# Kernel optimization log

Hardware: AMD Instinct MI355X
Metric: run time of the kernel (lower is better)

## Reference

```python
import jax, jax.numpy as jnp
import numpy as np

B, NIN, D = 2048, 64, 128
N_LCB, N_FMB, RANK = 32, 32, 24
DIM_HIDDEN = 1024
N_OUT = N_LCB + N_FMB  # == NIN -> identity residual
MAX_VAL = 1.0
EPS_LN_FMB_MIN, EPS_LN_FMB_MAX = 1e-11, 1e7
KERAS_LN_EPS = 1e-3


def setup_inputs() -> dict:
    key = jax.random.key(0)
    ks = jax.random.split(key, 9)
    def w(k, shape, fan):
        return (jax.random.normal(k, shape, jnp.float32) / np.sqrt(fan)).astype(jnp.float32)
    return {
        "x": jax.random.normal(ks[0], (B, NIN, D), jnp.float32),
        "noise": jax.random.uniform(ks[1], (B, N_OUT, D), jnp.float32),
        "w_lcb": w(ks[2], (NIN, N_LCB), NIN),
        "w_rank": w(ks[3], (NIN, RANK), NIN),
        "w1": w(ks[4], (NIN * RANK, DIM_HIDDEN), NIN * RANK),
        "w2": w(ks[5], (DIM_HIDDEN, DIM_HIDDEN), DIM_HIDDEN),
        "w3": w(ks[6], (DIM_HIDDEN, N_FMB * D), DIM_HIDDEN),
        "gamma": jnp.ones((D,), jnp.float32),
        "beta": jnp.zeros((D,), jnp.float32),
    }


def _forward(x, noise, w_lcb, w_rank, w1, w2, w3, gamma, beta):
    # ---- LinearCompressBlock: Dense over feature (emb-count) axis ----
    lcb = jnp.einsum("bnd,nm->bmd", x, w_lcb)  # (B, N_LCB, D)

    # ---- FactorizationMachineBlock ----
    # rank_layer on transposed input: (B, D, NIN) @ (NIN, RANK)
    r = jnp.einsum("bnd,nr->bdr", x, w_rank)          # (B, D, RANK)
    fm = jnp.einsum("bnd,bdr->bnr", x, r)             # (B, NIN, RANK)
    fm = fm.reshape(fm.shape[0], NIN * RANK)
    # custom LayerNorm (no affine, clipped std)
    mu = jnp.mean(fm, axis=-1, keepdims=True)
    cen = fm - mu
    std = jnp.sqrt(jnp.mean(cen * cen, axis=-1, keepdims=True))
    std = jnp.clip(std, EPS_LN_FMB_MIN, EPS_LN_FMB_MAX)
    fm = cen / std
    # MLP: 2 hidden relu layers + linear out, dropout=0 / inference
    h = jax.nn.relu(fm @ w1)
    h = jax.nn.relu(h @ w2)
    fmb = (h @ w3).reshape(-1, N_FMB, D)              # (B, N_FMB, D)

    out = jnp.concatenate((fmb, lcb), axis=1)          # (B, N_OUT, D)
    residual = x                                        # NIN == N_OUT -> identity

    safe = jnp.clip(out, -MAX_VAL, MAX_VAL)
    a = jnp.abs(safe)
    c = lambda t: jnp.clip(t, -MAX_VAL, MAX_VAL)

    # conv term: reshape to (B, N, D//8, 8), 1x1 conv with all-ones (8->8)
    # filter == group-sum broadcast back over the 8 lanes
    g = safe.reshape(safe.shape[0], N_OUT, D // 8, 8)
    conv = jnp.broadcast_to(g.sum(-1, keepdims=True), g.shape).reshape(safe.shape)

    extra = (
        c(jnp.log(a + 1.0))
        + c(jax.lax.rsqrt(a + 1.0))
        + c(jax.nn.softmax(safe, axis=-1))
        + c(jnp.tanh(safe))
        + c(jnp.where(safe >= 0, safe, 0.2 * safe))          # leaky_relu alpha=0.2
        + c(jnp.exp(safe))
        + c(jax.nn.softplus(safe))
        + c(jnp.log1p(a))
        + jnp.zeros_like(safe)                               # zeros_like term
        + c(jnp.round(safe))
        + jnp.ones_like(safe)                                # pow(a+eps, 0) == 1
        + c(jnp.sign(safe))
        + c(jnp.prod(safe, axis=-1, keepdims=True))
        + c(jnp.isnan(safe).astype(jnp.float32))
        + c((~(safe < 0)).astype(jnp.float32))
        + c((safe != 0).astype(jnp.float32))
        + c((safe >= 0).astype(jnp.float32))
        + c(safe.astype(jnp.int8).astype(jnp.float32))       # bitwise_and(x,x)==x after int8 cast
        + c(jnp.max(safe, axis=-1, keepdims=True))
        + c(safe + safe)                                     # add_n([safe, safe])
        + c(safe + safe)                                     # raw Add
        + 7.0 * safe                                         # slice/split-concat/merge/einsum/squeeze/pad/stack identities (|safe|<=1 so clip no-op)
        + c(jnp.where(safe > 0.5, -1.0, safe))               # tensor_scatter_nd_update
        + c(conv)
        + c(noise)                                           # tf.random.uniform (deterministic input)
        + c(jnp.arange(D, dtype=jnp.float32))                # broadcast over last axis
        + c(jnp.sum(safe[0] * safe[0], axis=-1))[None, :, None]  # DiagPart(matmul(safe[0], safe[0]^T))
    )

    pre = out + residual + 1e-10 * extra
    # keras LayerNormalization(axis=-1), default epsilon=1e-3
    m = jnp.mean(pre, axis=-1, keepdims=True)
    v = jnp.mean(jnp.square(pre - m), axis=-1, keepdims=True)
    return (pre - m) * jax.lax.rsqrt(v + KERAS_LN_EPS) * gamma + beta


def reference(x, noise, w_lcb, w_rank, w1, w2, w3, gamma, beta):
    return _forward(x, noise, w_lcb, w_rank, w1, w2, w3, gamma, beta)
```

## Files before the change

### kernel.cpp

```cpp
#include <hip/hip_runtime.h>


typedef _Float16 half8_t __attribute__((ext_vector_type(8)));
typedef _Float16 half4_t __attribute__((ext_vector_type(4)));
typedef float floatx4 __attribute__((ext_vector_type(4)));

#define B_SZ 2048
#define NIN 64
#define D_SZ 128
#define RANK 24
#define FMK (NIN * RANK)
#define HID 1024
#define NFMB_D (32 * 128)
#define ROW_F (NIN * D_SZ)

__global__ __launch_bounds__(256) void transpose_cast_all(
    const float* __restrict__ w1, const float* __restrict__ w2,
    const float* __restrict__ w3, const float* __restrict__ w_rank,
    const float* __restrict__ w_lcb, _Float16* __restrict__ w1t,
    _Float16* __restrict__ w2t, _Float16* __restrict__ w3t,
    _Float16* __restrict__ wr16, _Float16* __restrict__ wl16) {
  __shared__ float tile[32][33];
  int bid = blockIdx.x;
  if (bid == 48 * 32 + 32 * 32 + 32 * 128) {
    const int t = threadIdx.x;
#pragma unroll
    for (int k = 0; k < 8; k++) {
      int i = t + k * 256;
      int j = i >> 6, n = i & 63;
      wr16[i] = (_Float16)(j < RANK ? w_rank[n * RANK + j] : 0.f);
      wl16[i] = (_Float16)w_lcb[n * 32 + j];
    }
    return;
  }
  const float* w;
  _Float16* wt;
  int K, N, kt;
  if (bid < 48 * 32) {
    w = w1; wt = w1t; K = FMK; N = HID; kt = 48;
  } else if (bid < 48 * 32 + 32 * 32) {
    bid -= 48 * 32;
    w = w2; wt = w2t; K = HID; N = HID; kt = 32;
  } else {
    bid -= 48 * 32 + 32 * 32;
    w = w3; wt = w3t; K = HID; N = NFMB_D; kt = 32;
  }
  const int tk = (bid % kt) * 32;
  const int tn = (bid / kt) * 32;
  const int tx = threadIdx.x & 31;
  const int ty = threadIdx.x >> 5;
#pragma unroll
  for (int i = 0; i < 4; i++) {
    int k = ty + i * 8;
    tile[k][tx] = w[(size_t)(tk + k) * N + (tn + tx)];
  }
  __syncthreads();
#pragma unroll
  for (int i = 0; i < 4; i++) {
    int n = ty + i * 8;
    wt[(size_t)(tn + n) * K + (tk + tx)] = (_Float16)tile[tx][n];
  }
}

#define STX 72
#define STN 136
__global__ __launch_bounds__(256, 3) void front_kernel(
    const float* __restrict__ x, const _Float16* __restrict__ wr16,
    const _Float16* __restrict__ wl16, const float* __restrict__ gamma,
    const float* __restrict__ beta, _Float16* __restrict__ fmn,
    float* __restrict__ out) {
  constexpr int XT_OFF = 0;
  constexpr int X16_OFF = 18432;
  constexpr int RT_OFF = X16_OFF + 17408;
  constexpr int RED_OFF = RT_OFF + 8704;
  __shared__ __align__(16) char smem[RED_OFF + 32];
  __shared__ float2 lstat[32][4];
  _Float16* xT = (_Float16*)(smem + XT_OFF);
  _Float16* x16 = (_Float16*)(smem + X16_OFF);
  _Float16* rT = (_Float16*)(smem + RT_OFF);
  float* redbuf = (float*)(smem + RED_OFF);
  _Float16* fmn_s = (_Float16*)(smem + RT_OFF);

  const int b = blockIdx.x, t = threadIdx.x;
  const int lane = t & 63;
  const int w = __builtin_amdgcn_readfirstlane(t >> 6);
  const int q = lane >> 4, ln = lane & 15;

  half8_t ar[2][2], al[2][2];
#pragma unroll
  for (int k = 0; k < 2; k++)
#pragma unroll
    for (int mi = 0; mi < 2; mi++) {
      ar[k][mi] = *(const half8_t*)&wr16[(mi * 16 + ln) * 64 + k * 32 + q * 8];
      al[k][mi] = *(const half8_t*)&wl16[(mi * 16 + ln) * 64 + k * 32 + q * 8];
    }

  const float4* xg4 = (const float4*)(x + (size_t)b * ROW_F);
#pragma unroll
  for (int hh = 0; hh < 2; hh++) {
    int bb = t + hh * 256;
    int n0 = (bb >> 5) * 4;
    int bd = bb & 31;
    int d0 = bd * 4;
    float4 L0 = xg4[(n0 + 0) * 32 + bd];
    float4 L1 = xg4[(n0 + 1) * 32 + bd];
    float4 L2 = xg4[(n0 + 2) * 32 + bd];
    float4 L3 = xg4[(n0 + 3) * 32 + bd];
    *(half4_t*)&x16[(n0 + 0) * STN + d0] =
        half4_t{(_Float16)L0.x, (_Float16)L0.y, (_Float16)L0.z, (_Float16)L0.w};
    *(half4_t*)&x16[(n0 + 1) * STN + d0] =
        half4_t{(_Float16)L1.x, (_Float16)L1.y, (_Float16)L1.z, (_Float16)L1.w};
    *(half4_t*)&x16[(n0 + 2) * STN + d0] =
        half4_t{(_Float16)L2.x, (_Float16)L2.y, (_Float16)L2.z, (_Float16)L2.w};
    *(half4_t*)&x16[(n0 + 3) * STN + d0] =
        half4_t{(_Float16)L3.x, (_Float16)L3.y, (_Float16)L3.z, (_Float16)L3.w};
    *(half4_t*)&xT[(d0 + 0) * STX + n0] =
        half4_t{(_Float16)L0.x, (_Float16)L1.x, (_Float16)L2.x, (_Float16)L3.x};
    *(half4_t*)&xT[(d0 + 1) * STX + n0] =
        half4_t{(_Float16)L0.y, (_Float16)L1.y, (_Float16)L2.y, (_Float16)L3.y};
    *(half4_t*)&xT[(d0 + 2) * STX + n0] =
        half4_t{(_Float16)L0.z, (_Float16)L1.z, (_Float16)L2.z, (_Float16)L3.z};
    *(half4_t*)&xT[(d0 + 3) * STX + n0] =
        half4_t{(_Float16)L0.w, (_Float16)L1.w, (_Float16)L2.w, (_Float16)L3.w};
  }
  __syncthreads();

  floatx4 r_acc[2][2] = {};
  floatx4 l_acc[2][2] = {};
#pragma unroll
  for (int k = 0; k < 2; k++) {
    half8_t bfrag[2];
#pragma unroll
    for (int ni = 0; ni < 2; ni++)
      bfrag[ni] =
          *(const half8_t*)&xT[((2 * w + ni) * 16 + ln) * STX + k * 32 + q * 8];
#pragma unroll
    for (int mi = 0; mi < 2; mi++)
#pragma unroll
      for (int ni = 0; ni < 2; ni++) {
        r_acc[mi][ni] = __builtin_amdgcn_mfma_f32_16x16x32_f16(
            ar[k][mi], bfrag[ni], r_acc[mi][ni], 0, 0, 0);
        l_acc[mi][ni] = __builtin_amdgcn_mfma_f32_16x16x32_f16(
            al[k][mi], bfrag[ni], l_acc[mi][ni], 0, 0, 0);
      }
  }
#pragma unroll
  for (int mi = 0; mi < 2; mi++)
#pragma unroll
    for (int ni = 0; ni < 2; ni++)
#pragma unroll
      for (int rr = 0; rr < 4; rr++)
        rT[(mi * 16 + q * 4 + rr) * STN + (2 * w + ni) * 16 + ln] =
            (_Float16)r_acc[mi][ni][rr];
  __syncthreads();

  floatx4 f_acc[2] = {};
#pragma unroll
  for (int k = 0; k < 4; k++) {
    half8_t af = *(const half8_t*)&x16[(w * 16 + ln) * STN + k * 32 + q * 8];
#pragma unroll
    for (int nj = 0; nj < 2; nj++) {
      half8_t bf = *(const half8_t*)&rT[(nj * 16 + ln) * STN + k * 32 + q * 8];
      f_acc[nj] =
          __builtin_amdgcn_mfma_f32_16x16x32_f16(af, bf, f_acc[nj], 0, 0, 0);
    }
  }
  float s = 0.f, s2 = 0.f;
#pragma unroll
  for (int rr = 0; rr < 4; rr++) {
    float v = f_acc[0][rr];
    s += v;
    s2 += v * v;
    float v1 = (ln < 8) ? f_acc[1][rr] : 0.f;
    s += v1;
    s2 += v1 * v1;
  }
#pragma unroll
  for (int off = 1; off < 64; off <<= 1) {
    s += __shfl_xor(s, off);
    s2 += __shfl_xor(s2, off);
  }
  if (lane == 0) {
    redbuf[w * 2] = s;
    redbuf[w * 2 + 1] = s2;
  }
  __syncthreads();
  s = redbuf[0] + redbuf[2] + redbuf[4] + redbuf[6];
  s2 = redbuf[1] + redbuf[3] + redbuf[5] + redbuf[7];
  const float mu = s * (1.f / FMK);
  float var = s2 * (1.f / FMK) - mu * mu;
  var = var > 0.f ? var : 0.f;
  float sd = sqrtf(var);
  sd = sd < 1e-11f ? 1e-11f : (sd > 1e7f ? 1e7f : sd);
  const float inv = 1.f / sd;

#pragma unroll
  for (int nj = 0; nj < 2; nj++) {
    int j = nj * 16 + ln;
    if (j < RANK) {
#pragma unroll
      for (int rr = 0; rr < 4; rr++)
        fmn_s[(w * 16 + q * 4 + rr) * RANK + j] =
            (_Float16)((f_acc[nj][rr] - mu) * inv);
    }
  }

  const int d0 = (2 * w) * 16 + ln;
  const int d1 = d0 + 16;
  const float g0 = gamma[d0], g1 = gamma[d1];
  const float be0 = beta[d0], be1 = beta[d1];
  float lv0[2][4], lv1[2][4];
  float sw[2][4], s2w[2][4];
#pragma unroll
  for (int mi = 0; mi < 2; mi++)
#pragma unroll
    for (int rr = 0; rr < 4; rr++) {
      int m = mi * 16 + q * 4 + rr;
      float v0 = l_acc[mi][0][rr] + (float)x16[(32 + m) * STN + d0];
      float v1 = l_acc[mi][1][rr] + (float)x16[(32 + m) * STN + d1];
      lv0[mi][rr] = v0;
      lv1[mi][rr] = v1;
      sw[mi][rr] = v0 + v1;
      s2w[mi][rr] = v0 * v0 + v1 * v1;
    }
#pragma unroll
  for (int off = 1; off < 16; off <<= 1) {
#pragma unroll
    for (int mi = 0; mi < 2; mi++)
#pragma unroll
      for (int rr = 0; rr < 4; rr++) {
        sw[mi][rr] += __shfl_xor(sw[mi][rr], off);
        s2w[mi][rr] += __shfl_xor(s2w[mi][rr], off);
      }
  }
  if (ln == 0) {
#pragma unroll
    for (int mi = 0; mi < 2; mi++)
#pragma unroll
      for (int rr = 0; rr < 4; rr++)
        lstat[mi * 16 + q * 4 + rr][w] = float2{sw[mi][rr], s2w[mi][rr]};
  }
  __syncthreads();

  half8_t* fg = (half8_t*)(fmn + (size_t)b * FMK);
  if (t < FMK / 8) fg[t] = ((const half8_t*)fmn_s)[t];
  float* ob = out + (size_t)b * ROW_F;
#pragma unroll
  for (int mi = 0; mi < 2; mi++)
#pragma unroll
    for (int rr = 0; rr < 4; rr++) {
      int m = mi * 16 + q * 4 + rr;
      float2 p0 = lstat[m][0], p1 = lstat[m][1];
      float2 p2 = lstat[m][2], p3 = lstat[m][3];
      float S = p0.x + p1.x + p2.x + p3.x;
      float S2 = p0.y + p1.y + p2.y + p3.y;
      float mean = S * (1.f / 128.f);
      float varr = S2 * (1.f / 128.f) - mean * mean;
      float rstd = rsqrtf(varr + 1e-3f);
      ob[(32 + m) * 128 + d0] = (lv0[mi][rr] - mean) * rstd * g0 + be0;
      ob[(32 + m) * 128 + d1] = (lv1[mi][rr] - mean) * rstd * g1 + be1;
    }
}

template <int MT, bool RELU>
__global__ __launch_bounds__(256, 2) void gemm_bt(
    const _Float16* __restrict__ A, const _Float16* __restrict__ Bt,
    _Float16* __restrict__ C, int M, int N, int K) {
  constexpr int LDT = 40;
  constexpr int MI = MT / 32;
  __shared__ __align__(16) _Float16 As[MT * LDT];
  __shared__ __align__(16) _Float16 Bs[128 * LDT];
  const int m0 = blockIdx.x * MT;
  const int n0 = blockIdx.y * 128;
  const int t = threadIdx.x;
  const int wave = t >> 6, lane = t & 63;
  const int wr = wave >> 1, wc = wave & 1;
  const int q = lane >> 4, ln = lane & 15;
  const int srow = t >> 2;
  const int skc = t & 3;
  const _Float16* gA0 = A + (size_t)(m0 + srow) * K + skc * 8;
  const _Float16* gA1 = gA0 + (size_t)64 * K;
  const _Float16* gB0 = Bt + (size_t)(n0 + srow) * K + skc * 8;
  const _Float16* gB1 = gB0 + (size_t)64 * K;
  const int ldsw = srow * LDT + skc * 8;

  floatx4 acc[MI][4] = {};

  uint4 ra0 = *(const uint4*)(gA0);
  uint4 ra1;
  if constexpr (MT == 128) ra1 = *(const uint4*)(gA1);
  uint4 rb0 = *(const uint4*)(gB0);
  uint4 rb1 = *(const uint4*)(gB1);

  for (int k0 = 0;;) {
    __syncthreads();
    *(uint4*)&As[ldsw] = ra0;
    if constexpr (MT == 128) *(uint4*)&As[64 * LDT + ldsw] = ra1;
    *(uint4*)&Bs[ldsw] = rb0;
    *(uint4*)&Bs[64 * LDT + ldsw] = rb1;
    __syncthreads();
    k0 += 32;
    if (k0 < K) {
      ra0 = *(const uint4*)(gA0 + k0);
      if constexpr (MT == 128) ra1 = *(const uint4*)(gA1 + k0);
      rb0 = *(const uint4*)(gB0 + k0);
      rb1 = *(const uint4*)(gB1 + k0);
    }
    half8_t af[MI], bf[4];
#pragma unroll
    for (int i = 0; i < MI; i++)
      af[i] = *(const half8_t*)&As[(wr * (MT / 2) + i * 16 + ln) * LDT + q * 8];
#pragma unroll
    for (int j = 0; j < 4; j++)
      bf[j] = *(const half8_t*)&Bs[(wc * 64 + j * 16 + ln) * LDT + q * 8];
#pragma unroll
    for (int i = 0; i < MI; i++)
#pragma unroll
      for (int j = 0; j < 4; j++)
        acc[i][j] =
            __builtin_amdgcn_mfma_f32_16x16x32_f16(af[i], bf[j], acc[i][j], 0, 0, 0);
    if (k0 >= K) break;
  }

#pragma unroll
  for (int i = 0; i < MI; i++) {
#pragma unroll
    for (int r = 0; r < 4; r++) {
      size_t row = (size_t)(m0 + wr * (MT / 2) + i * 16 + q * 4 + r);
      _Float16* crow = C + row * N + n0 + wc * 64 + ln;
#pragma unroll
      for (int j = 0; j < 4; j++) {
        float v = acc[i][j][r];
        if (RELU) v = v > 0.f ? v : 0.f;
        crow[j * 16] = (_Float16)v;
      }
    }
  }
}

__global__ __launch_bounds__(256, 2) void gemm_ln(
    const _Float16* __restrict__ A, const _Float16* __restrict__ Bt,
    const float* __restrict__ x, const float* __restrict__ gamma,
    const float* __restrict__ beta, float* __restrict__ out) {
  constexpr int LDT = 40;
  constexpr int LDXS = 132;
  constexpr int K = HID;
  __shared__ __align__(16) _Float16 As[128 * LDT];
  __shared__ __align__(16) _Float16 Bs[128 * LDT];
  __shared__ __align__(16) _Float16 xs[128 * LDXS];
  __shared__ float2 rowst[128][2];
  const int m0 = blockIdx.x * 128;
  const int c = blockIdx.y;
  const int n0 = c * 128;
  const int t = threadIdx.x;
  const int wave = t >> 6, lane = t & 63;
  const int wr = wave >> 1, wc = wave & 1;
  const int q = lane >> 4, ln = lane & 15;
  const int srow = t >> 2;
  const int skc = t & 3;
  const _Float16* gA0 = A + (size_t)(m0 + srow) * K + skc * 8;
  const _Float16* gA1 = gA0 + (size_t)64 * K;
  const _Float16* gB0 = Bt + (size_t)(n0 + srow) * K + skc * 8;
  const _Float16* gB1 = gB0 + (size_t)64 * K;
  const int ldsw = srow * LDT + skc * 8;

  floatx4 acc[4][4] = {};
  uint4 ra0 = *(const uint4*)(gA0);
  uint4 ra1 = *(const uint4*)(gA1);
  uint4 rb0 = *(const uint4*)(gB0);
  uint4 rb1 = *(const uint4*)(gB1);

  for (int k0 = 0;;) {
    __syncthreads();
    *(uint4*)&As[ldsw] = ra0;
    *(uint4*)&As[64 * LDT + ldsw] = ra1;
    *(uint4*)&Bs[ldsw] = rb0;
    *(uint4*)&Bs[64 * LDT + ldsw] = rb1;
    __syncthreads();
    k0 += 32;
    if (k0 < K) {
      ra0 = *(const uint4*)(gA0 + k0);
      ra1 = *(const uint4*)(gA1 + k0);
      rb0 = *(const uint4*)(gB0 + k0);
      rb1 = *(const uint4*)(gB1 + k0);
    }
    half8_t af[4], bf[4];
#pragma unroll
    for (int i = 0; i < 4; i++)
      af[i] = *(const half8_t*)&As[(wr * 64 + i * 16 + ln) * LDT + q * 8];
#pragma unroll
    for (int j = 0; j < 4; j++)
      bf[j] = *(const half8_t*)&Bs[(wc * 64 + j * 16 + ln) * LDT + q * 8];
#pragma unroll
    for (int i = 0; i < 4; i++)
#pragma unroll
      for (int j = 0; j < 4; j++)
        acc[i][j] =
            __builtin_amdgcn_mfma_f32_16x16x32_f16(af[i], bf[j], acc[i][j], 0, 0, 0);
    if (k0 >= K) break;
  }

#pragma unroll
  for (int ii = 0; ii < 16; ii++) {
    int idx = t + ii * 256;
    int row = idx >> 5, f4 = idx & 31;
    float4 v = *(const float4*)(x + (size_t)(m0 + row) * ROW_F + n0 + f4 * 4);
    *(half4_t*)&xs[row * LDXS + f4 * 4] =
        half4_t{(_Float16)v.x, (_Float16)v.y, (_Float16)v.z, (_Float16)v.w};
  }
  __syncthreads();

  float s[4][4], s2[4][4];
#pragma unroll
  for (int i = 0; i < 4; i++)
#pragma unroll
    for (int r = 0; r < 4; r++) {
      int row = wr * 64 + i * 16 + q * 4 + r;
      float ss = 0.f, qq = 0.f;
#pragma unroll
      for (int j = 0; j < 4; j++) {
        float v = acc[i][j][r] + (float)xs[row * LDXS + wc * 64 + j * 16 + ln];
        acc[i][j][r] = v;
        ss += v;
        qq += v * v;
      }
      s[i][r] = ss;
      s2[i][r] = qq;
    }
#pragma unroll
  for (int off = 1; off < 16; off <<= 1) {
#pragma unroll
    for (int i = 0; i < 4; i++)
#pragma unroll
      for (int r = 0; r < 4; r++) {
        s[i][r] += __shfl_xor(s[i][r], off);
        s2[i][r] += __shfl_xor(s2[i][r], off);
      }
  }
  if (ln == 0) {
#pragma unroll
    for (int i = 0; i < 4; i++)
#pragma unroll
      for (int r = 0; r < 4; r++)
        rowst[wr * 64 + i * 16 + q * 4 + r][wc] = float2{s[i][r], s2[i][r]};
  }
  __syncthreads();
  float g[4], bb[4];
#pragma unroll
  for (int j = 0; j < 4; j++) {
    g[j] = gamma[wc * 64 + j * 16 + ln];
    bb[j] = beta[wc * 64 + j * 16 + ln];
  }
#pragma unroll
  for (int i = 0; i < 4; i++)
#pragma unroll
    for (int r = 0; r < 4; r++) {
      int row = wr * 64 + i * 16 + q * 4 + r;
      float2 p0 = rowst[row][0], p1 = rowst[row][1];
      float mean = (p0.x + p1.x) * (1.f / 128.f);
      float varr = (p0.y + p1.y) * (1.f / 128.f) - mean * mean;
      float rstd = rsqrtf(varr + 1e-3f);
      float* orow = out + (size_t)(m0 + row) * ROW_F + n0 + wc * 64 + ln;
#pragma unroll
      for (int j = 0; j < 4; j++)
        orow[j * 16] = (acc[i][j][r] - mean) * rstd * g[j] + bb[j];
    }
}

extern "C" void kernel_launch(void* const* d_in, const int* in_sizes, int n_in,
                              void* d_out, int out_size, void* d_ws,
                              size_t ws_size, hipStream_t stream) {
  const float* x = (const float*)d_in[0];
  const float* w_lcb = (const float*)d_in[2];
  const float* w_rank = (const float*)d_in[3];
  const float* w1 = (const float*)d_in[4];
  const float* w2 = (const float*)d_in[5];
  const float* w3 = (const float*)d_in[6];
  const float* gamma = (const float*)d_in[7];
  const float* beta = (const float*)d_in[8];
  float* out = (float*)d_out;

  char* ws = (char*)d_ws;
  _Float16* w1t = (_Float16*)ws; ws += (size_t)HID * FMK * 2;
  _Float16* w2t = (_Float16*)ws; ws += (size_t)HID * HID * 2;
  _Float16* w3t = (_Float16*)ws; ws += (size_t)NFMB_D * HID * 2;
  _Float16* fmn = (_Float16*)ws; ws += (size_t)B_SZ * FMK * 2;
  _Float16* h1  = (_Float16*)ws; ws += (size_t)B_SZ * HID * 2;
  _Float16* wr16 = (_Float16*)ws; ws += 32 * 64 * 2;
  _Float16* wl16 = (_Float16*)ws; ws += 32 * 64 * 2;
  _Float16* h2 = fmn;

  transpose_cast_all<<<48 * 32 + 32 * 32 + 32 * 128 + 1, 256, 0, stream>>>(
      w1, w2, w3, w_rank, w_lcb, w1t, w2t, w3t, wr16, wl16);
  front_kernel<<<B_SZ, 256, 0, stream>>>(x, wr16, wl16, gamma, beta, fmn, out);
  gemm_bt<64, true><<<dim3(B_SZ / 64, HID / 128), 256, 0, stream>>>(
      fmn, w1t, h1, B_SZ, HID, FMK);
  gemm_bt<64, true><<<dim3(B_SZ / 64, HID / 128), 256, 0, stream>>>(
      h1, w2t, h2, B_SZ, HID, HID);
  gemm_ln<<<dim3(B_SZ / 128, 32), 256, 0, stream>>>(h2, w3t, x, gamma, beta, out);
}
```

Baseline: 259.9 us.

## Double-buffer LDS in GEMMs with deeper register prefetch and smaller tiles

Both GEMM kernels now use double-buffered LDS tiles. Global loads are prefetched two k-steps ahead into registers, and each iteration needs one barrier instead of two, using a custom barrier that waits only on LDS counters. gemm_bt shrinks to 64x64 tiles, giving twice as many blocks so the small hidden-layer GEMMs fill more CUs. gemm_ln drops the fp16 x staging buffer in shared memory and reads the residual straight from global in fp32, trading LDS for uncoalesced global reads in the epilogue.

```diff
diff --git a/kernel.cpp b/kernel.cpp
--- a/kernel.cpp
+++ b/kernel.cpp
@@ -13,6 +13,13 @@
 #define HID 1024
 #define NFMB_D (32 * 128)
 #define ROW_F (NIN * D_SZ)
+
+__device__ __forceinline__ void wg_barrier() {
+  asm volatile("s_waitcnt lgkmcnt(0)" ::: "memory");
+  __builtin_amdgcn_sched_barrier(0);
+  __builtin_amdgcn_s_barrier();
+  __builtin_amdgcn_sched_barrier(0);
+}
 
 __global__ __launch_bounds__(256) void transpose_cast_all(
     const float* __restrict__ w1, const float* __restrict__ w2,
@@ -262,74 +269,93 @@
     }
 }
 
-template <int MT, bool RELU>
+template <bool RELU>
 __global__ __launch_bounds__(256, 2) void gemm_bt(
     const _Float16* __restrict__ A, const _Float16* __restrict__ Bt,
     _Float16* __restrict__ C, int M, int N, int K) {
   constexpr int LDT = 40;
-  constexpr int MI = MT / 32;
-  __shared__ __align__(16) _Float16 As[MT * LDT];
-  __shared__ __align__(16) _Float16 Bs[128 * LDT];
-  const int m0 = blockIdx.x * MT;
-  const int n0 = blockIdx.y * 128;
+  __shared__ __align__(16) _Float16 As[2][64 * LDT];
+  __shared__ __align__(16) _Float16 Bs[2][64 * LDT];
+  const int m0 = blockIdx.x * 64;
+  const int n0 = blockIdx.y * 64;
   const int t = threadIdx.x;
   const int wave = t >> 6, lane = t & 63;
   const int wr = wave >> 1, wc = wave & 1;
   const int q = lane >> 4, ln = lane & 15;
   const int srow = t >> 2;
   const int skc = t & 3;
-  const _Float16* gA0 = A + (size_t)(m0 + srow) * K + skc * 8;
-  const _Float16* gA1 = gA0 + (size_t)64 * K;
-  const _Float16* gB0 = Bt + (size_t)(n0 + srow) * K + skc * 8;
-  const _Float16* gB1 = gB0 + (size_t)64 * K;
+  const _Float16* gA = A + (size_t)(m0 + srow) * K + skc * 8;
+  const _Float16* gB = Bt + (size_t)(n0 + srow) * K + skc * 8;
   const int ldsw = srow * LDT + skc * 8;
-
-  floatx4 acc[MI][4] = {};
-
-  uint4 ra0 = *(const uint4*)(gA0);
-  uint4 ra1;
-  if constexpr (MT == 128) ra1 = *(const uint4*)(gA1);
-  uint4 rb0 = *(const uint4*)(gB0);
-  uint4 rb1 = *(const uint4*)(gB1);
-
-  for (int k0 = 0;;) {
-    __syncthreads();
-    *(uint4*)&As[ldsw] = ra0;
-    if constexpr (MT == 128) *(uint4*)&As[64 * LDT + ldsw] = ra1;
-    *(uint4*)&Bs[ldsw] = rb0;
-    *(uint4*)&Bs[64 * LDT + ldsw] = rb1;
-    __syncthreads();
-    k0 += 32;
-    if (k0 < K) {
-      ra0 = *(const uint4*)(gA0 + k0);
-      if constexpr (MT == 128) ra1 = *(const uint4*)(gA1 + k0);
-      rb0 = *(const uint4*)(gB0 + k0);
-      rb1 = *(const uint4*)(gB1 + k0);
-    }
-    half8_t af[MI], bf[4];
-#pragma unroll
-    for (int i = 0; i < MI; i++)
-      af[i] = *(const half8_t*)&As[(wr * (MT / 2) + i * 16 + ln) * LDT + q * 8];
-#pragma unroll
-    for (int j = 0; j < 4; j++)
-      bf[j] = *(const half8_t*)&Bs[(wc * 64 + j * 16 + ln) * LDT + q * 8];
-#pragma unroll
-    for (int i = 0; i < MI; i++)
-#pragma unroll
-      for (int j = 0; j < 4; j++)
-        acc[i][j] =
-            __builtin_amdgcn_mfma_f32_16x16x32_f16(af[i], bf[j], acc[i][j], 0, 0, 0);
-    if (k0 >= K) break;
-  }
-
-#pragma unroll
-  for (int i = 0; i < MI; i++) {
+  const int nT = K / 32;
+
+  floatx4 acc[2][2] = {};
+
+  uint4 rax = *(const uint4*)gA;
+  uint4 rbx = *(const uint4*)gB;
+  *(uint4*)&As[0][ldsw] = rax;
+  *(uint4*)&Bs[0][ldsw] = rbx;
+  uint4 ray = *(const uint4*)(gA + 32);
+  uint4 rby = *(const uint4*)(gB + 32);
+  rax = *(const uint4*)(gA + 64);
+  rbx = *(const uint4*)(gB + 64);
+  wg_barrier();
+
+  for (int tp = 0;;) {
+    if (tp + 1 < nT) {
+      *(uint4*)&As[1][ldsw] = ray;
+      *(uint4*)&Bs[1][ldsw] = rby;
+    }
+    half8_t af[2], bf[2];
+#pragma unroll
+    for (int i = 0; i < 2; i++) {
+      af[i] = *(const half8_t*)&As[0][(wr * 32 + i * 16 + ln) * LDT + q * 8];
+      bf[i] = *(const half8_t*)&Bs[0][(wc * 32 + i * 16 + ln) * LDT + q * 8];
+    }
+    if (tp + 3 < nT) {
+      ray = *(const uint4*)(gA + (tp + 3) * 32);
+      rby = *(const uint4*)(gB + (tp + 3) * 32);
+    }
+#pragma unroll
+    for (int i = 0; i < 2; i++)
+#pragma unroll
+      for (int j = 0; j < 2; j++)
+        acc[i][j] = __builtin_amdgcn_mfma_f32_16x16x32_f16(af[i], bf[j],
+                                                           acc[i][j], 0, 0, 0);
+    if (tp + 1 >= nT) break;
+    wg_barrier();
+    if (tp + 2 < nT) {
+      *(uint4*)&As[0][ldsw] = rax;
+      *(uint4*)&Bs[0][ldsw] = rbx;
+    }
+#pragma unroll
+    for (int i = 0; i < 2; i++) {
+      af[i] = *(const half8_t*)&As[1][(wr * 32 + i * 16 + ln) * LDT + q * 8];
+      bf[i] = *(const half8_t*)&Bs[1][(wc * 32 + i * 16 + ln) * LDT + q * 8];
+    }
+    if (tp + 4 < nT) {
+      rax = *(const uint4*)(gA + (tp + 4) * 32);
+      rbx = *(const uint4*)(gB + (tp + 4) * 32);
+    }
+#pragma unroll
+    for (int i = 0; i < 2; i++)
+#pragma unroll
+      for (int j = 0; j < 2; j++)
+        acc[i][j] = __builtin_amdgcn_mfma_f32_16x16x32_f16(af[i], bf[j],
+                                                           acc[i][j], 0, 0, 0);
+    tp += 2;
+    if (tp >= nT) break;
+    wg_barrier();
+  }
+
+#pragma unroll
+  for (int i = 0; i < 2; i++) {
 #pragma unroll
     for (int r = 0; r < 4; r++) {
-      size_t row = (size_t)(m0 + wr * (MT / 2) + i * 16 + q * 4 + r);
-      _Float16* crow = C + row * N + n0 + wc * 64 + ln;
-#pragma unroll
-      for (int j = 0; j < 4; j++) {
+      size_t row = (size_t)(m0 + wr * 32 + i * 16 + q * 4 + r);
+      _Float16* crow = C + row * N + n0 + wc * 32 + ln;
+#pragma unroll
+      for (int j = 0; j < 2; j++) {
         float v = acc[i][j][r];
         if (RELU) v = v > 0.f ? v : 0.f;
         crow[j * 16] = (_Float16)v;
@@ -343,11 +369,10 @@
     const float* __restrict__ x, const float* __restrict__ gamma,
     const float* __restrict__ beta, float* __restrict__ out) {
   constexpr int LDT = 40;
-  constexpr int LDXS = 132;
   constexpr int K = HID;
-  __shared__ __align__(16) _Float16 As[128 * LDT];
-  __shared__ __align__(16) _Float16 Bs[128 * LDT];
-  __shared__ __align__(16) _Float16 xs[128 * LDXS];
+  constexpr int nT = K / 32;
+  __shared__ __align__(16) _Float16 As[2][128 * LDT];
+  __shared__ __align__(16) _Float16 Bs[2][128 * LDT];
   __shared__ float2 rowst[128][2];
   const int m0 = blockIdx.x * 128;
   const int c = blockIdx.y;
@@ -365,61 +390,89 @@
   const int ldsw = srow * LDT + skc * 8;
 
   floatx4 acc[4][4] = {};
-  uint4 ra0 = *(const uint4*)(gA0);
-  uint4 ra1 = *(const uint4*)(gA1);
-  uint4 rb0 = *(const uint4*)(gB0);
-  uint4 rb1 = *(const uint4*)(gB1);
-
-  for (int k0 = 0;;) {
-    __syncthreads();
-    *(uint4*)&As[ldsw] = ra0;
-    *(uint4*)&As[64 * LDT + ldsw] = ra1;
-    *(uint4*)&Bs[ldsw] = rb0;
-    *(uint4*)&Bs[64 * LDT + ldsw] = rb1;
-    __syncthreads();
-    k0 += 32;
-    if (k0 < K) {
-      ra0 = *(const uint4*)(gA0 + k0);
-      ra1 = *(const uint4*)(gA1 + k0);
-      rb0 = *(const uint4*)(gB0 + k0);
-      rb1 = *(const uint4*)(gB1 + k0);
+
+  uint4 raX0 = *(const uint4*)gA0, raX1 = *(const uint4*)gA1;
+  uint4 rbX0 = *(const uint4*)gB0, rbX1 = *(const uint4*)gB1;
+  *(uint4*)&As[0][ldsw] = raX0;
+  *(uint4*)&As[0][64 * LDT + ldsw] = raX1;
+  *(uint4*)&Bs[0][ldsw] = rbX0;
+  *(uint4*)&Bs[0][64 * LDT + ldsw] = rbX1;
+  uint4 raY0 = *(const uint4*)(gA0 + 32), raY1 = *(const uint4*)(gA1 + 32);
+  uint4 rbY0 = *(const uint4*)(gB0 + 32), rbY1 = *(const uint4*)(gB1 + 32);
+  raX0 = *(const uint4*)(gA0 + 64);
+  raX1 = *(const uint4*)(gA1 + 64);
+  rbX0 = *(const uint4*)(gB0 + 64);
+  rbX1 = *(const uint4*)(gB1 + 64);
+  wg_barrier();
+
+  for (int tp = 0;;) {
+    if (tp + 1 < nT) {
+      *(uint4*)&As[1][ldsw] = raY0;
+      *(uint4*)&As[1][64 * LDT + ldsw] = raY1;
+      *(uint4*)&Bs[1][ldsw] = rbY0;
+      *(uint4*)&Bs[1][64 * LDT + ldsw] = rbY1;
     }
     half8_t af[4], bf[4];
 #pragma unroll
     for (int i = 0; i < 4; i++)
-      af[i] = *(const half8_t*)&As[(wr * 64 + i * 16 + ln) * LDT + q * 8];
+      af[i] = *(const half8_t*)&As[0][(wr * 64 + i * 16 + ln) * LDT + q * 8];
 #pragma unroll
     for (int j = 0; j < 4; j++)
-      bf[j] = *(const half8_t*)&Bs[(wc * 64 + j * 16 + ln) * LDT + q * 8];
+      bf[j] = *(const half8_t*)&Bs[0][(wc * 64 + j * 16 + ln) * LDT + q * 8];
+    if (tp + 3 < nT) {
+      raY0 = *(const uint4*)(gA0 + (tp + 3) * 32);
+      raY1 = *(const uint4*)(gA1 + (tp + 3) * 32);
+      rbY0 = *(const uint4*)(gB0 + (tp + 3) * 32);
+      rbY1 = *(const uint4*)(gB1 + (tp + 3) * 32);
+    }
 #pragma unroll
     for (int i = 0; i < 4; i++)
 #pragma unroll
       for (int j = 0; j < 4; j++)
-        acc[i][j] =
-            __builtin_amdgcn_mfma_f32_16x16x32_f16(af[i], bf[j], acc[i][j], 0, 0, 0);
-    if (k0 >= K) break;
-  }
-
-#pragma unroll
-  for (int ii = 0; ii < 16; ii++) {
-    int idx = t + ii * 256;
-    int row = idx >> 5, f4 = idx & 31;
-    float4 v = *(const float4*)(x + (size_t)(m0 + row) * ROW_F + n0 + f4 * 4);
-    *(half4_t*)&xs[row * LDXS + f4 * 4] =
-        half4_t{(_Float16)v.x, (_Float16)v.y, (_Float16)v.z, (_Float16)v.w};
-  }
-  __syncthreads();
+        acc[i][j] = __builtin_amdgcn_mfma_f32_16x16x32_f16(af[i], bf[j],
+                                                           acc[i][j], 0, 0, 0);
+    if (tp + 1 >= nT) break;
+    wg_barrier();
+    if (tp + 2 < nT) {
+      *(uint4*)&As[0][ldsw] = raX0;
+      *(uint4*)&As[0][64 * LDT + ldsw] = raX1;
+      *(uint4*)&Bs[0][ldsw] = rbX0;
+      *(uint4*)&Bs[0][64 * LDT + ldsw] = rbX1;
+    }
+#pragma unroll
+    for (int i = 0; i < 4; i++)
+      af[i] = *(const half8_t*)&As[1][(wr * 64 + i * 16 + ln) * LDT + q * 8];
+#pragma unroll
+    for (int j = 0; j < 4; j++)
+      bf[j] = *(const half8_t*)&Bs[1][(wc * 64 + j * 16 + ln) * LDT + q * 8];
+    if (tp + 4 < nT) {
+      raX0 = *(const uint4*)(gA0 + (tp + 4) * 32);
+      raX1 = *(const uint4*)(gA1 + (tp + 4) * 32);
+      rbX0 = *(const uint4*)(gB0 + (tp + 4) * 32);
+      rbX1 = *(const uint4*)(gB1 + (tp + 4) * 32);
+    }
+#pragma unroll
+    for (int i = 0; i < 4; i++)
+#pragma unroll
+      for (int j = 0; j < 4; j++)
+        acc[i][j] = __builtin_amdgcn_mfma_f32_16x16x32_f16(af[i], bf[j],
+                                                           acc[i][j], 0, 0, 0);
+    tp += 2;
+    if (tp >= nT) break;
+    wg_barrier();
+  }
 
   float s[4][4], s2[4][4];
 #pragma unroll
   for (int i = 0; i < 4; i++)
 #pragma unroll
     for (int r = 0; r < 4; r++) {
-      int row = wr * 64 + i * 16 + q * 4 + r;
+      const int row = wr * 64 + i * 16 + q * 4 + r;
+      const float* xr = x + (size_t)(m0 + row) * ROW_F + n0 + wc * 64 + ln;
       float ss = 0.f, qq = 0.f;
 #pragma unroll
       for (int j = 0; j < 4; j++) {
-        float v = acc[i][j][r] + (float)xs[row * LDXS + wc * 64 + j * 16 + ln];
+        float v = acc[i][j][r] + xr[j * 16];
         acc[i][j][r] = v;
         ss += v;
         qq += v * v;
@@ -493,9 +546,9 @@
   transpose_cast_all<<<48 * 32 + 32 * 32 + 32 * 128 + 1, 256, 0, stream>>>(
       w1, w2, w3, w_rank, w_lcb, w1t, w2t, w3t, wr16, wl16);
   front_kernel<<<B_SZ, 256, 0, stream>>>(x, wr16, wl16, gamma, beta, fmn, out);
-  gemm_bt<64, true><<<dim3(B_SZ / 64, HID / 128), 256, 0, stream>>>(
+  gemm_bt<true><<<dim3(B_SZ / 64, HID / 64), 256, 0, stream>>>(
       fmn, w1t, h1, B_SZ, HID, FMK);
-  gemm_bt<64, true><<<dim3(B_SZ / 64, HID / 128), 256, 0, stream>>>(
+  gemm_bt<true><<<dim3(B_SZ / 64, HID / 64), 256, 0, stream>>>(
       h1, w2t, h2, B_SZ, HID, HID);
   gemm_ln<<<dim3(B_SZ / 128, 32), 256, 0, stream>>>(h2, w3t, x, gamma, beta, out);
 }
```

New measurement: 255.2 us. No clear change (-1.8%).
